# Performance work log

Measured on AMD Instinct MI355X. Metric: run time of the kernel, lower is better.

## Reference

```python
import jax, jax.numpy as jnp
import numpy as np
import math

B, T, C = 1, 2048, 2048
N_HEAD = 32
N_QUERY_GROUPS = 8
HEAD_SIZE = 64
ROPE_N_ELEM = 16  # int(0.25 * 64)
Q_PER_KV = N_HEAD // N_QUERY_GROUPS  # 4
QKV_DIM = (N_HEAD + 2 * N_QUERY_GROUPS) * HEAD_SIZE  # 3072


def setup_inputs() -> dict:
    key = jax.random.key(0)
    ks = jax.random.split(key, 7)
    x = jax.random.normal(ks[0], (B, T, C), dtype=jnp.float32)
    # realistic rope tables
    inv_freq = 1.0 / (10000.0 ** (jnp.arange(0, ROPE_N_ELEM, 2, dtype=jnp.float32) / ROPE_N_ELEM))
    t = jnp.arange(T, dtype=jnp.float32)
    freqs = jnp.outer(t, inv_freq)                       # [T, rope/2]
    emb = jnp.concatenate([freqs, freqs], axis=-1)       # [T, rope]
    cos, sin = jnp.cos(emb), jnp.sin(emb)
    s = 0.02
    W_attn = jax.random.normal(ks[1], (QKV_DIM, C), dtype=jnp.float32) * s
    b_attn = jax.random.normal(ks[2], (QKV_DIM,), dtype=jnp.float32) * s
    W_proj = jax.random.normal(ks[3], (C, N_HEAD * HEAD_SIZE), dtype=jnp.float32) * s
    b_proj = jax.random.normal(ks[4], (C,), dtype=jnp.float32) * s
    return {"x": x, "cos": cos, "sin": sin, "W_attn": W_attn, "b_attn": b_attn,
            "W_proj": W_proj, "b_proj": b_proj}


def _apply_rope(t, cos, sin):
    # t: [B, H, T, rope]; cos/sin: [T, rope]
    half = t.shape[-1] // 2
    t1, t2 = t[..., :half], t[..., half:]
    rotated = jnp.concatenate([-t2, t1], axis=-1)
    return t * cos + rotated * sin


def reference(x, cos, sin, W_attn, b_attn, W_proj, b_proj):
    Bc, Tc, Cc = x.shape
    qkv = x @ W_attn.T + b_attn                                   # [B, T, 3072]
    qkv = qkv.reshape(Bc, Tc, N_QUERY_GROUPS, Q_PER_KV + 2, HEAD_SIZE)
    qkv = qkv.transpose(0, 2, 3, 1, 4)                            # [B, G, q_per_kv+2, T, hs]
    q = qkv[:, :, :Q_PER_KV]                                      # [B, G, q_per_kv, T, hs]
    k = qkv[:, :, Q_PER_KV:Q_PER_KV + 1]                          # [B, G, 1, T, hs]
    v = qkv[:, :, Q_PER_KV + 1:]
    # GQA expand (n_query_groups != n_head, prefill path)
    k = jnp.broadcast_to(k, (Bc, N_QUERY_GROUPS, Q_PER_KV, Tc, HEAD_SIZE))
    v = jnp.broadcast_to(v, (Bc, N_QUERY_GROUPS, Q_PER_KV, Tc, HEAD_SIZE))
    q = q.reshape(Bc, N_HEAD, Tc, HEAD_SIZE)
    k = k.reshape(Bc, N_HEAD, Tc, HEAD_SIZE)
    v = v.reshape(Bc, N_HEAD, Tc, HEAD_SIZE)
    # partial RoPE on first ROPE_N_ELEM dims
    q = jnp.concatenate([_apply_rope(q[..., :ROPE_N_ELEM], cos, sin), q[..., ROPE_N_ELEM:]], axis=-1)
    k = jnp.concatenate([_apply_rope(k[..., :ROPE_N_ELEM], cos, sin), k[..., ROPE_N_ELEM:]], axis=-1)
    # causal SDPA with scale 1/sqrt(head_size)
    scale = 1.0 / math.sqrt(HEAD_SIZE)
    scores = jnp.einsum('bhqd,bhkd->bhqk', q, k) * scale          # [B, H, T, T]
    causal = jnp.tril(jnp.ones((Tc, Tc), dtype=bool))
    scores = jnp.where(causal, scores, jnp.finfo(scores.dtype).min)
    attn = jax.nn.softmax(scores, axis=-1)
    y = jnp.einsum('bhqk,bhkd->bhqd', attn, v)                    # [B, H, T, hs]
    y = y.transpose(0, 2, 1, 3).reshape(Bc, Tc, N_HEAD * HEAD_SIZE)
    return y @ W_proj.T + b_proj
```

## Files before the change

### kernel.cpp

```cpp
#include <hip/hip_runtime.h>
#include <hip/hip_bf16.h>

using u16 = unsigned short;
typedef float f32x4 __attribute__((ext_vector_type(4)));
typedef __bf16 bf16x8 __attribute__((ext_vector_type(8)));

#define T_SEQ 2048
#define C_DIM 2048
#define QKV_DIM 3072
#define N_HEAD 32
#define N_GROUPS 8
#define HEAD_SIZE 64
#define ROPE_N 16
#define NEG_BIG (-1e30f)
#define LSP 76
#define QSCALE 0.18033688011112043f

__device__ inline float bf2f(u16 u) {
    union { float f; unsigned v; } x; x.v = ((unsigned)u) << 16; return x.f;
}
__device__ inline u16 f2bf(float f) {
    __bf16 h = (__bf16)f;
    return *(u16*)&h;
}
__device__ inline int4 cvt8(int4 lo, int4 hi) {
    const float* fa = (const float*)&lo;
    const float* fb = (const float*)&hi;
    __attribute__((aligned(16))) u16 o[8] = {
        f2bf(fa[0]), f2bf(fa[1]), f2bf(fa[2]), f2bf(fa[3]),
        f2bf(fb[0]), f2bf(fb[1]), f2bf(fb[2]), f2bf(fb[3]) };
    return *(const int4*)o;
}

__device__ __forceinline__ int detect_fp32(const unsigned* __restrict__ xw) {
    int cnt = 0;
#pragma unroll
    for (int i = 0; i < 128; i++) {
        unsigned w = xw[i];
        cnt += (((w >> 7)  & 0xFF) >= 0xC0);
        cnt += (((w >> 23) & 0xFF) >= 0xC0);
    }
    return cnt > 8;
}

__device__ __forceinline__ void gl_lds16(const u16* g, u16* l) {
    __builtin_amdgcn_global_load_lds(
        (const __attribute__((address_space(1))) unsigned int*)g,
        (__attribute__((address_space(3))) unsigned int*)l,
        16, 0, 0);
}

struct ConvDesc {
    const void* src[7];
    u16*        dst[7];
    int         off8[8];
};

__global__ void convert_all(ConvDesc cd)
{
    const int fl = detect_fp32((const unsigned*)cd.src[0]);
    int gid = blockIdx.x * blockDim.x + threadIdx.x;
    if (gid >= cd.off8[7]) return;
    int seg = 0;
#pragma unroll
    for (int s = 1; s < 7; s++) seg += (gid >= cd.off8[s]);
    int i = (gid - cd.off8[seg]) * 8;
    if (fl) {
        const float4* s = (const float4*)((const float*)cd.src[seg] + i);
        *(int4*)(cd.dst[seg] + i) = cvt8(*(const int4*)&s[0], *(const int4*)&s[1]);
    } else {
        *(int4*)(cd.dst[seg] + i) = *(const int4*)((const u16*)cd.src[seg] + i);
    }
}

__global__ __launch_bounds__(256) void gemm_qkv_rope(
    const u16* __restrict__ A, const u16* __restrict__ W,
    const u16* __restrict__ bias,
    const u16* __restrict__ ccos, const u16* __restrict__ csin,
    u16* __restrict__ Qout, u16* __restrict__ Kout, u16* __restrict__ Vtout)
{
    __shared__ __attribute__((aligned(16))) u16 lds_a[2][64 * 64];
    __shared__ __attribute__((aligned(16))) u16 lds_b[2][128 * 64];

    const int tid  = threadIdx.x;
    const int wave = tid >> 6;
    const int lane = tid & 63;
    const int quad = lane >> 4;
    const int l16  = lane & 15;
    const int bm = blockIdx.y * 64;
    const int bn = blockIdx.x * 128;
    const int K = C_DIM;

    f32x4 acc[4][2] = {};

    int srow[4], sgc[4];
#pragma unroll
    for (int k = 0; k < 4; k++) {
        int s = tid + k * 256;
        srow[k] = s >> 3;
        sgc[k]  = (s & 7) ^ (srow[k] & 7);
    }
    const int xh = l16 & 7;

    auto stage = [&](int k0, int p) {
#pragma unroll
        for (int k = 0; k < 2; k++) {
            int s = tid + k * 256;
            gl_lds16(A + (size_t)(bm + srow[k]) * K + k0 + sgc[k] * 8, lds_a[p] + s * 8);
        }
#pragma unroll
        for (int k = 0; k < 4; k++) {
            int s = tid + k * 256;
            gl_lds16(W + (size_t)(bn + srow[k]) * K + k0 + sgc[k] * 8, lds_b[p] + s * 8);
        }
    };

    stage(0, 0);
    const int nsteps = K / 64;
    for (int kt = 0; kt < nsteps; kt++) {
        const int p = kt & 1;
        __syncthreads();
        if (kt + 1 < nsteps) stage((kt + 1) * 64, p ^ 1);

        bf16x8 afr[4][2], bfr[2][2];
#pragma unroll
        for (int ks = 0; ks < 2; ks++) {
            int c = ((ks * 4 + quad) ^ xh) * 8;
#pragma unroll
            for (int i = 0; i < 4; i++)
                afr[i][ks] = *(const bf16x8*)(lds_a[p] + (i * 16 + l16) * 64 + c);
#pragma unroll
            for (int j = 0; j < 2; j++)
                bfr[j][ks] = *(const bf16x8*)(lds_b[p] + (wave * 32 + j * 16 + l16) * 64 + c);
        }
#pragma unroll
        for (int ks = 0; ks < 2; ks++)
#pragma unroll
            for (int i = 0; i < 4; i++)
#pragma unroll
                for (int j = 0; j < 2; j++)
                    acc[i][j] = __builtin_amdgcn_mfma_f32_16x16x32_bf16(afr[i][ks], bfr[j][ks], acc[i][j], 0, 0, 0);
    }

#pragma unroll
    for (int j = 0; j < 2; j++) {
        const int colb = bn + wave * 32 + j * 16;
        const int col  = colb + l16;
        const int slot = (colb % 384) >> 6;
        const int g    = colb / 384;
        const int dbase = colb & 63;
        const int d    = dbase + l16;
        const float bv = bf2f(bias[col]);
        const bool rope = (dbase == 0) && (slot != 5);
#pragma unroll
        for (int i = 0; i < 4; i++) {
            const int trow = bm + i * 16 + quad * 4;
#pragma unroll
            for (int r = 0; r < 4; r++) {
                float v = acc[i][j][r] + bv;
                float outv = v;
                if (rope) {
                    float part = __shfl_xor(v, 8, 64);
                    float rot = (l16 < 8) ? -part : part;
                    float cc = bf2f(ccos[(trow + r) * ROPE_N + l16]);
                    float ss = bf2f(csin[(trow + r) * ROPE_N + l16]);
                    outv = v * cc + rot * ss;
                }
                const int t = trow + r;
                if (slot < 4) {
                    int hh = g * 4 + slot;
                    Qout[((size_t)hh * T_SEQ + t) * 64 + d] = f2bf(outv * QSCALE);
                } else if (slot == 4) {
                    Kout[((size_t)g * T_SEQ + t) * 64 + d] = f2bf(outv);
                } else {
                    Vtout[((size_t)g * 64 + d) * T_SEQ + t] = f2bf(outv);
                }
            }
        }
    }
}

__global__ __launch_bounds__(256) void gemm_bt(
    const u16* __restrict__ A, const u16* __restrict__ W,
    const u16* __restrict__ bias, u16* __restrict__ Cout,
    int M, int N, int K, const unsigned* __restrict__ xprobe)
{
    __shared__ __attribute__((aligned(16))) u16 lds_a[2][64 * 64];
    __shared__ __attribute__((aligned(16))) u16 lds_b[2][64 * 64];

    const int tid  = threadIdx.x;
    const int wave = tid >> 6;
    const int lane = tid & 63;
    const int quad = lane >> 4;
    const int l16  = lane & 15;
    const int bm = blockIdx.y * 64;
    const int bn = blockIdx.x * 64;
    const int fl = detect_fp32(xprobe);

    f32x4 acc[4] = {};

    int srow[2], sgc[2];
#pragma unroll
    for (int k = 0; k < 2; k++) {
        int s = tid + k * 256;
        srow[k] = s >> 3;
        sgc[k]  = (s & 7) ^ (srow[k] & 7);
    }
    const int xh = l16 & 7;

    auto stage = [&](int k0, int p) {
#pragma unroll
        for (int k = 0; k < 2; k++) {
            int s = tid + k * 256;
            gl_lds16(A + (size_t)(bm + srow[k]) * K + k0 + sgc[k] * 8, lds_a[p] + s * 8);
            gl_lds16(W + (size_t)(bn + srow[k]) * K + k0 + sgc[k] * 8, lds_b[p] + s * 8);
        }
    };

    stage(0, 0);
    const int nsteps = K / 64;
    for (int kt = 0; kt < nsteps; kt++) {
        const int p = kt & 1;
        __syncthreads();
        if (kt + 1 < nsteps) stage((kt + 1) * 64, p ^ 1);

        bf16x8 afr[4][2], bfr[2];
#pragma unroll
        for (int ks = 0; ks < 2; ks++) {
            int c = ((ks * 4 + quad) ^ xh) * 8;
#pragma unroll
            for (int i = 0; i < 4; i++)
                afr[i][ks] = *(const bf16x8*)(lds_a[p] + (i * 16 + l16) * 64 + c);
            bfr[ks] = *(const bf16x8*)(lds_b[p] + (wave * 16 + l16) * 64 + c);
        }
#pragma unroll
        for (int ks = 0; ks < 2; ks++)
#pragma unroll
            for (int i = 0; i < 4; i++)
                acc[i] = __builtin_amdgcn_mfma_f32_16x16x32_bf16(afr[i][ks], bfr[ks], acc[i], 0, 0, 0);
    }

    const int col = bn + wave * 16 + l16;
    const float bv = bf2f(bias[col]);
#pragma unroll
    for (int i = 0; i < 4; i++) {
        int row = bm + i * 16 + quad * 4;
#pragma unroll
        for (int r = 0; r < 4; r++) {
            float v = acc[i][r] + bv;
            size_t idx = (size_t)(row + r) * N + col;
            if (fl) ((float*)Cout)[idx] = v;
            else    Cout[idx] = f2bf(v);
        }
    }
}

__global__ __launch_bounds__(256) void flash_attn(
    const u16* __restrict__ Q, const u16* __restrict__ K,
    const u16* __restrict__ Vt, u16* __restrict__ Y)
{
    __shared__ __attribute__((aligned(16))) u16 lds_q[64 * 64];
    __shared__ __attribute__((aligned(16))) u16 lds_k[2][64 * 64];
    __shared__ __attribute__((aligned(16))) u16 lds_vt[2][64 * 64];
    __shared__ __attribute__((aligned(16))) u16 lds_p[4][16 * LSP];

    const int h  = blockIdx.y;
    const int g  = h >> 2;
    const int tid  = threadIdx.x;
    const int wave = tid >> 6;
    const int lane = tid & 63;
    const int quad = lane >> 4;
    const int l16  = lane & 15;
    const int NQT = T_SEQ / 64;

    const u16* Qh = Q  + (size_t)h * T_SEQ * 64;
    const u16* Kg = K  + (size_t)g * T_SEQ * 64;
    const u16* Vg = Vt + (size_t)g * 64 * T_SEQ;

    const int srow = tid >> 3;
    const int sgc  = (tid & 7) ^ (srow & 7);
    const int xh   = l16 & 7;

    bf16x8 vones;
#pragma unroll
    for (int i = 0; i < 8; i++) vones[i] = (__bf16)1.0f;

    int4 kr0, kr1, vr0, vr1;
    auto load_tile = [&](int k0) {
        kr0 = *(const int4*)(Kg + (size_t)(k0 + srow) * 64 + sgc * 8);
        kr1 = *(const int4*)(Kg + (size_t)(k0 + srow + 32) * 64 + sgc * 8);
        vr0 = *(const int4*)(Vg + (size_t)srow * T_SEQ + k0 + sgc * 8);
        vr1 = *(const int4*)(Vg + (size_t)(srow + 32) * T_SEQ + k0 + sgc * 8);
    };

    for (int pass = 0; pass < 2; pass++) {
        const int qt = pass ? (NQT - 1 - blockIdx.x) : blockIdx.x;
        const int q0 = qt * 64;

        __syncthreads();
#pragma unroll
        for (int k = 0; k < 2; k++) {
            int s = tid + k * 256;
            int row = srow + k * 32;
            *(int4*)(lds_q + s * 8) =
                *(const int4*)(Qh + (size_t)(q0 + row) * 64 + sgc * 8);
        }
        __syncthreads();

        bf16x8 a_q[2];
#pragma unroll
        for (int ks = 0; ks < 2; ks++)
            a_q[ks] = *(const bf16x8*)(lds_q + (wave * 16 + l16) * 64 + (((ks * 4 + quad) ^ xh) * 8));

        f32x4 o_acc[4] = {};
        f32x4 acc_l = {};

        load_tile(0);

        for (int kt = 0; kt <= qt; kt++) {
            const int p = kt & 1;
            *(int4*)(lds_k[p]  + tid * 8)         = kr0;
            *(int4*)(lds_k[p]  + (tid + 256) * 8) = kr1;
            *(int4*)(lds_vt[p] + tid * 8)         = vr0;
            *(int4*)(lds_vt[p] + (tid + 256) * 8) = vr1;
            __syncthreads();
            if (kt < qt) load_tile((kt + 1) * 64);

            f32x4 sc[4] = {};
#pragma unroll
            for (int ks = 0; ks < 2; ks++) {
                int c = ((ks * 4 + quad) ^ xh) * 8;
#pragma unroll
                for (int t = 0; t < 4; t++) {
                    bf16x8 bk = *(const bf16x8*)(lds_k[p] + (t * 16 + l16) * 64 + c);
                    sc[t] = __builtin_amdgcn_mfma_f32_16x16x32_bf16(a_q[ks], bk, sc[t], 0, 0, 0);
                }
            }

            if (kt == qt) {
                const int row_g = q0 + wave * 16 + quad * 4;
                const int k0 = kt * 64;
#pragma unroll
                for (int t = 0; t < 4; t++) {
                    int col_g = k0 + t * 16 + l16;
#pragma unroll
                    for (int r = 0; r < 4; r++)
                        if (col_g > row_g + r) sc[t][r] = NEG_BIG;
                }
            }

#pragma unroll
            for (int t = 0; t < 4; t++) {
                int colo = t * 16 + l16;
#pragma unroll
                for (int r = 0; r < 4; r++) {
                    float pv = __builtin_amdgcn_exp2f(sc[t][r]);
                    lds_p[wave][(quad * 4 + r) * LSP + colo] = f2bf(pv);
                }
            }

#pragma unroll
            for (int ks = 0; ks < 2; ks++) {
                int c = ((ks * 4 + quad) ^ xh) * 8;
                bf16x8 apf = *(const bf16x8*)(lds_p[wave] + l16 * LSP + ks * 32 + quad * 8);
#pragma unroll
                for (int t = 0; t < 4; t++) {
                    bf16x8 bvf = *(const bf16x8*)(lds_vt[p] + (t * 16 + l16) * 64 + c);
                    o_acc[t] = __builtin_amdgcn_mfma_f32_16x16x32_bf16(apf, bvf, o_acc[t], 0, 0, 0);
                }
                acc_l = __builtin_amdgcn_mfma_f32_16x16x32_bf16(apf, vones, acc_l, 0, 0, 0);
            }
        }

#pragma unroll
        for (int t = 0; t < 4; t++)
#pragma unroll
            for (int r = 0; r < 4; r++) {
                int row = q0 + wave * 16 + quad * 4 + r;
                int d   = t * 16 + l16;
                Y[(size_t)row * (N_HEAD * HEAD_SIZE) + h * 64 + d] = f2bf(o_acc[t][r] / acc_l[r]);
            }
    }
}

extern "C" void kernel_launch(void* const* d_in, const int* in_sizes, int n_in,
                              void* d_out, int out_size, void* d_ws, size_t ws_size,
                              hipStream_t stream)
{
    u16* base = (u16*)d_ws;

    u16* cx   = base;
    u16* cWa  = cx  + (size_t)T_SEQ * C_DIM;
    u16* cba  = cWa + (size_t)QKV_DIM * C_DIM;
    u16* cWp  = cba + QKV_DIM;
    u16* cbp  = cWp + (size_t)C_DIM * C_DIM;
    u16* ccos = cbp + C_DIM;
    u16* csin = ccos + (size_t)T_SEQ * ROPE_N;
    u16* Qb   = csin + (size_t)T_SEQ * ROPE_N;
    u16* Kb   = Qb + (size_t)N_HEAD * T_SEQ * HEAD_SIZE;
    u16* Vtb  = Kb + (size_t)N_GROUPS * T_SEQ * HEAD_SIZE;
    u16* Yb   = Vtb + (size_t)N_GROUPS * T_SEQ * HEAD_SIZE;

    dim3 blk(256);

    ConvDesc cd;
    const int sizes[7] = { T_SEQ * C_DIM, T_SEQ * ROPE_N, T_SEQ * ROPE_N,
                           QKV_DIM * C_DIM, QKV_DIM, C_DIM * C_DIM, C_DIM };
    u16* dsts[7] = { cx, ccos, csin, cWa, cba, cWp, cbp };
    int acc8 = 0;
    for (int i = 0; i < 7; i++) {
        cd.src[i] = d_in[i];
        cd.dst[i] = dsts[i];
        cd.off8[i] = acc8;
        acc8 += sizes[i] / 8;
    }
    cd.off8[7] = acc8;
    convert_all<<<dim3((acc8 + 255) / 256), blk, 0, stream>>>(cd);

    gemm_qkv_rope<<<dim3(QKV_DIM / 128, T_SEQ / 64), blk, 0, stream>>>(
        cx, cWa, cba, ccos, csin, Qb, Kb, Vtb);
    flash_attn<<<dim3(T_SEQ / 128, N_HEAD), blk, 0, stream>>>(Qb, Kb, Vtb, Yb);
    gemm_bt<<<dim3(C_DIM / 64, T_SEQ / 64), blk, 0, stream>>>(
        Yb, cWp, cbp, (u16*)d_out, T_SEQ, C_DIM, N_HEAD * HEAD_SIZE,
        (const unsigned*)d_in[0]);
}
```

Measured before the change: 247.0 us.

## Replace LDS staging in gemm_bt with direct global-to-register double buffering

The GEMM no longer stages A and W tiles through shared memory with async global-to-LDS copies and barriers. Each wave now loads its MFMA fragments straight from global memory into registers, ping-ponging two register buffers so the next tile's loads overlap the current MFMAs. Launch bounds now also request 4 blocks per CU. This removes LDS traffic and __syncthreads, but each of the 4 waves re-reads the same A rows from global memory (4x redundant A traffic, served by cache) using strided, less coalesced 16-byte loads, and register pressure grows.

Result: slower. 355.8 us (+44.0%).

```diff
diff --git a/kernel.cpp b/kernel.cpp
--- a/kernel.cpp
+++ b/kernel.cpp
@@ -180,14 +180,11 @@
     }
 }
 
-__global__ __launch_bounds__(256) void gemm_bt(
+__global__ __launch_bounds__(256, 4) void gemm_bt(
     const u16* __restrict__ A, const u16* __restrict__ W,
     const u16* __restrict__ bias, u16* __restrict__ Cout,
     int M, int N, int K, const unsigned* __restrict__ xprobe)
 {
-    __shared__ __attribute__((aligned(16))) u16 lds_a[2][64 * 64];
-    __shared__ __attribute__((aligned(16))) u16 lds_b[2][64 * 64];
-
     const int tid  = threadIdx.x;
     const int wave = tid >> 6;
     const int lane = tid & 63;
@@ -199,45 +196,38 @@
 
     f32x4 acc[4] = {};
 
-    int srow[2], sgc[2];
-#pragma unroll
-    for (int k = 0; k < 2; k++) {
-        int s = tid + k * 256;
-        srow[k] = s >> 3;
-        sgc[k]  = (s & 7) ^ (srow[k] & 7);
-    }
-    const int xh = l16 & 7;
-
-    auto stage = [&](int k0, int p) {
-#pragma unroll
-        for (int k = 0; k < 2; k++) {
-            int s = tid + k * 256;
-            gl_lds16(A + (size_t)(bm + srow[k]) * K + k0 + sgc[k] * 8, lds_a[p] + s * 8);
-            gl_lds16(W + (size_t)(bn + srow[k]) * K + k0 + sgc[k] * 8, lds_b[p] + s * 8);
-        }
+    const u16* Abase = A + (size_t)(bm + l16) * K + quad * 8;
+    const u16* Wbase = W + (size_t)(bn + wave * 16 + l16) * K + quad * 8;
+
+    int4 bufA[10], bufB[10];
+    auto load_tile = [&](int k0, int4* dst) {
+#pragma unroll
+        for (int i = 0; i < 4; i++)
+#pragma unroll
+            for (int ks = 0; ks < 2; ks++)
+                dst[i * 2 + ks] = *(const int4*)(Abase + (size_t)(i * 16) * K + k0 + ks * 32);
+#pragma unroll
+        for (int ks = 0; ks < 2; ks++)
+            dst[8 + ks] = *(const int4*)(Wbase + k0 + ks * 32);
     };
-
-    stage(0, 0);
+    auto compute = [&](int4* buf) {
+#pragma unroll
+        for (int ks = 0; ks < 2; ks++) {
+            bf16x8 bv = *(const bf16x8*)&buf[8 + ks];
+#pragma unroll
+            for (int i = 0; i < 4; i++)
+                acc[i] = __builtin_amdgcn_mfma_f32_16x16x32_bf16(
+                    *(const bf16x8*)&buf[i * 2 + ks], bv, acc[i], 0, 0, 0);
+        }
+    };
+
     const int nsteps = K / 64;
-    for (int kt = 0; kt < nsteps; kt++) {
-        const int p = kt & 1;
-        __syncthreads();
-        if (kt + 1 < nsteps) stage((kt + 1) * 64, p ^ 1);
-
-        bf16x8 afr[4][2], bfr[2];
-#pragma unroll
-        for (int ks = 0; ks < 2; ks++) {
-            int c = ((ks * 4 + quad) ^ xh) * 8;
-#pragma unroll
-            for (int i = 0; i < 4; i++)
-                afr[i][ks] = *(const bf16x8*)(lds_a[p] + (i * 16 + l16) * 64 + c);
-            bfr[ks] = *(const bf16x8*)(lds_b[p] + (wave * 16 + l16) * 64 + c);
-        }
-#pragma unroll
-        for (int ks = 0; ks < 2; ks++)
-#pragma unroll
-            for (int i = 0; i < 4; i++)
-                acc[i] = __builtin_amdgcn_mfma_f32_16x16x32_bf16(afr[i][ks], bfr[ks], acc[i], 0, 0, 0);
+    load_tile(0, bufA);
+    for (int kt = 0; kt < nsteps; kt += 2) {
+        if (kt + 1 < nsteps) load_tile((kt + 1) * 64, bufB);
+        compute(bufA);
+        if (kt + 2 < nsteps) load_tile((kt + 2) * 64, bufA);
+        if (kt + 1 < nsteps) compute(bufB);
     }
 
     const int col = bn + wave * 16 + l16;
```
